# Kernel optimization log

Measured on AMD Instinct MI355X. Metric: run time of the kernel, lower is better.

Reference implementation:

```python
import jax, jax.numpy as jnp
import numpy as np

# Production-scale detection head dims
B_TOTAL = 16      # num_tbins(4) * batch_size(4)
NUM_ANCHORS = 100000
NUM_CLASSES = 8


def setup_inputs() -> dict:
    key = jax.random.key(0)
    k1, k2, k3, k4 = jax.random.split(key, 4)
    # anchors [A,4] = (cx, cy, w, h); widths/heights strictly positive
    ctr = jax.random.uniform(k1, (NUM_ANCHORS, 2), jnp.float32) * 512.0
    wh = jax.random.uniform(k2, (NUM_ANCHORS, 2), jnp.float32) * 64.0 + 8.0
    anchors = jnp.concatenate([ctr, wh], axis=-1)
    loc_preds = jax.random.normal(k3, (B_TOTAL, NUM_ANCHORS, 4), jnp.float32)
    # class scores in [0,1] (post-sigmoid semantics)
    cls_preds = jax.nn.sigmoid(jax.random.normal(k4, (B_TOTAL, NUM_ANCHORS, NUM_CLASSES), jnp.float32))
    return {
        "anchors": anchors,
        "loc_preds": loc_preds,
        "cls_preds": cls_preds,
        "varx": 0.1,
        "vary": 0.2,
        "score_thresh": 0.7,
        "batch_size": 4,
    }


def reference(anchors, loc_preds, cls_preds, varx, vary, score_thresh, batch_size):
    """Anchor decode + score-threshold filtering.

    Faithful to BoxDecoder.forward, but jit-compatible: instead of
    boolean-mask compaction into ragged per-(t,i) lists (data-dependent
    shapes), we return the dense [B*A*C, 6] box tensor plus the keep mask
    and batch_index; (mask, batch_index) fully determine the ragged
    targets[t][i] = box_tensor[mask & (batch_index == t*batch_size+i)].
    """
    B, A, C = cls_preds.shape
    # decode: xy = loc[:2]*varx*anchor_wh + anchor_xy ; wh = exp(loc[2:]*vary)*anchor_wh
    xy = loc_preds[..., :2] * varx * anchors[..., 2:] + anchors[..., :2]
    wh = jnp.exp(loc_preds[..., 2:] * vary) * anchors[..., 2:]
    box_preds = jnp.concatenate([xy - wh * 0.5, xy + wh * 0.5], axis=-1)  # [B,A,4]
    # expand boxes over classes, flatten to [B*A*C, ...] (same order as torch view(-1,...))
    boxes = jnp.broadcast_to(box_preds[:, :, None, :], (B, A, C, 4)).reshape(-1, 4)
    scores = cls_preds.reshape(-1)
    # idxs = b*C + c  ->  label = c+1, batch_index = b
    labels = jnp.broadcast_to(jnp.arange(C, dtype=jnp.float32) + 1.0, (B, A, C)).reshape(-1)
    batch_index = jnp.broadcast_to(jnp.arange(B, dtype=jnp.int32)[:, None, None], (B, A, C)).reshape(-1)
    box_tensor = jnp.concatenate([boxes, scores[:, None], labels[:, None]], axis=1)  # [B*A*C, 6]
    mask = scores >= score_thresh  # keep mask (compaction left to consumer / kernel)
    return box_tensor, mask, batch_index
```

## Files before the change

### kernel.cpp

```cpp
#include <hip/hip_runtime.h>
#include <math.h>


#define MAGIC_SHIFT 38

typedef float vfloat4 __attribute__((ext_vector_type(4)));

__global__ __launch_bounds__(256) void box_decode_pers(
    const vfloat4* __restrict__ anchors,
    const vfloat4* __restrict__ loc,
    const vfloat4* __restrict__ cls4,
    const float*   __restrict__ varx_p,
    const float*   __restrict__ vary_p,
    const float*   __restrict__ th_p,
    vfloat4*       __restrict__ out_box4,
    vfloat4*       __restrict__ out_mask4,
    vfloat4*       __restrict__ out_bidx4,
    unsigned nChunks, unsigned nT, unsigned A,
    unsigned long long invA)
{
    __shared__ vfloat4 s_box[4][64];
    __shared__ vfloat4 s_cls[4][128];

    const unsigned wv   = threadIdx.x >> 6;
    const unsigned lane = threadIdx.x & 63u;
    vfloat4* sbox  = s_box[wv];
    vfloat4* scls4 = s_cls[wv];
    const float* scls = (const float*)scls4;

    const float varx = *varx_p;
    const float vary = *vary_p;
    const float th   = *th_p;

    const unsigned gw = blockIdx.x * 4u + wv;
    const unsigned nw = gridDim.x * 4u;

    for (unsigned ch = gw; ch < nChunks; ch += nw) {
        const unsigned t0     = ch * 64u;
        const unsigned nt_blk = (nT - t0 < 64u) ? (nT - t0) : 64u;

        if (lane < nt_blk) {
            unsigned t = t0 + lane;
            unsigned b = (unsigned)(((unsigned long long)t * invA) >> MAGIC_SHIFT);
            unsigned a = t - b * A;
            vfloat4 anc = anchors[a];
            vfloat4 lp  = loc[t];
            float x = fmaf(lp.x * varx, anc.z, anc.x);
            float y = fmaf(lp.y * varx, anc.w, anc.y);
            float w = expf(lp.z * vary) * anc.z;
            float h = expf(lp.w * vary) * anc.w;
            vfloat4 bx;
            bx.x = fmaf(w, -0.5f, x);
            bx.y = fmaf(h, -0.5f, y);
            bx.z = fmaf(w,  0.5f, x);
            bx.w = fmaf(h,  0.5f, y);
            sbox[lane] = bx;
        }

        const unsigned cbase = t0 * 2u;
        const unsigned clim  = nt_blk * 2u;
        if (lane < clim) {
            vfloat4 c = cls4[cbase + lane];
            scls4[lane] = c;
            vfloat4 m;
            m.x = (c.x >= th) ? 1.0f : 0.0f;
            m.y = (c.y >= th) ? 1.0f : 0.0f;
            m.z = (c.z >= th) ? 1.0f : 0.0f;
            m.w = (c.w >= th) ? 1.0f : 0.0f;
            out_mask4[cbase + lane] = m;
            unsigned tm = t0 + (lane >> 1);
            unsigned bm = (unsigned)(((unsigned long long)tm * invA) >> MAGIC_SHIFT);
            float bf = (float)bm;
            vfloat4 bb = {bf, bf, bf, bf};
            out_bidx4[cbase + lane] = bb;
        }
        {
            unsigned l2 = lane + 64u;
            if (l2 < clim) {
                vfloat4 c = cls4[cbase + l2];
                scls4[l2] = c;
                vfloat4 m;
                m.x = (c.x >= th) ? 1.0f : 0.0f;
                m.y = (c.y >= th) ? 1.0f : 0.0f;
                m.z = (c.z >= th) ? 1.0f : 0.0f;
                m.w = (c.w >= th) ? 1.0f : 0.0f;
                out_mask4[cbase + l2] = m;
                unsigned tm = t0 + 32u + (lane >> 1);
                unsigned bm = (unsigned)(((unsigned long long)tm * invA) >> MAGIC_SHIFT);
                float bf = (float)bm;
                vfloat4 bb = {bf, bf, bf, bf};
                out_bidx4[cbase + l2] = bb;
            }
        }

        asm volatile("s_waitcnt lgkmcnt(0)" ::: "memory");

        const unsigned lim  = nt_blk * 12u;
        const unsigned base = t0 * 12u;
#pragma unroll
        for (unsigned k = 0u; k < 12u; ++k) {
            unsigned lg = k * 64u + lane;
            if (lg < lim) {
                unsigned lt = lg / 12u;
                unsigned j  = lg - lt * 12u;
                unsigned s  = j / 3u;
                unsigned jm = j - s * 3u;
                vfloat4 bx  = sbox[lt];
                float sc0 = scls[lt * 8u + 2u * s];
                float sc1 = scls[lt * 8u + 2u * s + 1u];
                float l0  = (float)(2u * s + 1u);
                float l1  = (float)(2u * s + 2u);
                bool j0 = (jm == 0u);
                bool j1 = (jm == 1u);
                vfloat4 r;
                r.x = j0 ? bx.x : (j1 ? sc0  : bx.z);
                r.y = j0 ? bx.y : (j1 ? l0   : bx.w);
                r.z = j0 ? bx.z : (j1 ? bx.x : sc1);
                r.w = j0 ? bx.w : (j1 ? bx.y : l1);
                out_box4[base + lg] = r;
            }
        }
    }
}

__global__ __launch_bounds__(256) void box_decode_kernel(
    const float4* __restrict__ anchors,
    const float4* __restrict__ loc,
    const float*  __restrict__ cls,
    const float*  __restrict__ varx_p,
    const float*  __restrict__ vary_p,
    const float*  __restrict__ th_p,
    vfloat4*      __restrict__ out_box4,
    float*        __restrict__ out_mask,
    float*        __restrict__ out_bidx,
    unsigned n4, unsigned A, unsigned C, unsigned f4_per_t,
    unsigned long long invA, unsigned long long invF)
{
    unsigned g = blockIdx.x * 256u + threadIdx.x;
    if (g >= n4) return;
    unsigned t  = (unsigned)(((unsigned long long)g * invF) >> MAGIC_SHIFT);
    unsigned j  = g - t * f4_per_t;
    unsigned b  = (unsigned)(((unsigned long long)t * invA) >> MAGIC_SHIFT);
    unsigned a  = t - b * A;
    unsigned s  = j / 3u;
    unsigned jm = j - s * 3u;
    float varx = *varx_p, vary = *vary_p, th = *th_p;
    float4 anc = anchors[a];
    float4 lp  = loc[t];
    float x = fmaf(lp.x * varx, anc.z, anc.x);
    float y = fmaf(lp.y * varx, anc.w, anc.y);
    float w = expf(lp.z * vary) * anc.z;
    float h = expf(lp.w * vary) * anc.w;
    float x1 = fmaf(w, -0.5f, x);
    float y1 = fmaf(h, -0.5f, y);
    float x2 = fmaf(w,  0.5f, x);
    float y2 = fmaf(h,  0.5f, y);
    unsigned r0 = t * C + 2u * s;
    float bf = (float)b;
    vfloat4 r;
    if (jm == 0u) {
        r.x = x1; r.y = y1; r.z = x2; r.w = y2;
    } else if (jm == 1u) {
        float sc0 = cls[r0];
        r.x = sc0; r.y = (float)(2u * s + 1u); r.z = x1; r.w = y1;
        out_mask[r0] = (sc0 >= th) ? 1.0f : 0.0f;
        out_bidx[r0] = bf;
    } else {
        float sc1 = cls[r0 + 1u];
        r.x = x2; r.y = y2; r.z = sc1; r.w = (float)(2u * s + 2u);
        out_mask[r0 + 1u] = (sc1 >= th) ? 1.0f : 0.0f;
        out_bidx[r0 + 1u] = bf;
    }
    out_box4[g] = r;
}

extern "C" void kernel_launch(void* const* d_in, const int* in_sizes, int n_in,
                              void* d_out, int out_size, void* d_ws, size_t ws_size,
                              hipStream_t stream) {
    const float* anchors = (const float*)d_in[0];
    const float* loc     = (const float*)d_in[1];
    const float* cls     = (const float*)d_in[2];
    const float* varx_p  = (const float*)d_in[3];
    const float* vary_p  = (const float*)d_in[4];
    const float* th_p    = (const float*)d_in[5];

    unsigned A = (unsigned)(in_sizes[0] / 4);
    unsigned B = (unsigned)((unsigned)in_sizes[1] / (4u * A));
    unsigned C = (unsigned)((unsigned)in_sizes[2] / (A * B));
    unsigned nT = B * A;
    unsigned rows = nT * C;

    float* out_box  = (float*)d_out;
    float* out_mask = out_box + (size_t)rows * 6;
    float* out_bidx = out_mask + rows;

    unsigned long long invA = ((1ULL << MAGIC_SHIFT) / A) + 1ULL;

    if (C == 8u) {
        unsigned nChunks = (nT + 63u) / 64u;
        unsigned nb = (nChunks + 3u) / 4u;
        if (nb > 2048u) nb = 2048u;
        box_decode_pers<<<dim3(nb), dim3(256), 0, stream>>>(
            (const vfloat4*)anchors, (const vfloat4*)loc, (const vfloat4*)cls,
            varx_p, vary_p, th_p,
            (vfloat4*)out_box, (vfloat4*)out_mask, (vfloat4*)out_bidx,
            nChunks, nT, A, invA);
    } else {
        unsigned f4_per_t = (6u * C) / 4u;
        unsigned n4 = rows * 6u / 4u;
        unsigned long long invF = ((1ULL << MAGIC_SHIFT) / f4_per_t) + 1ULL;
        unsigned nb = (n4 + 255u) / 256u;
        box_decode_kernel<<<dim3(nb), dim3(256), 0, stream>>>(
            (const float4*)anchors, (const float4*)loc, cls,
            varx_p, vary_p, th_p,
            (vfloat4*)out_box, out_mask, out_bidx,
            n4, A, C, f4_per_t, invA, invF);
    }
}
```

Before: 473.0 us.

## Split fused decode kernel into separate box, mask and batch-index kernels

Replaces the single persistent grid-stride kernel, which wrote boxes, mask and batch index together, with three launches: a non-persistent box kernel with one chunk per wave, a mask kernel that rereads the class scores, and a batch-index fill kernel. The intent is simpler per-kernel access patterns and a full-size grid instead of a 2048-block cap. In exchange the class scores are read twice from memory and there are two extra launch overheads on a bandwidth-bound workload.

```diff
diff --git a/kernel.cpp b/kernel.cpp
--- a/kernel.cpp
+++ b/kernel.cpp
@@ -6,16 +6,45 @@
 
 typedef float vfloat4 __attribute__((ext_vector_type(4)));
 
-__global__ __launch_bounds__(256) void box_decode_pers(
+__global__ __launch_bounds__(256) void bidx_kernel(
+    vfloat4* __restrict__ out_bidx4,
+    unsigned nf4, unsigned A,
+    unsigned long long invA)
+{
+    unsigned g = blockIdx.x * 256u + threadIdx.x;
+    if (g >= nf4) return;
+    unsigned t = g >> 1;
+    unsigned b = (unsigned)(((unsigned long long)t * invA) >> MAGIC_SHIFT);
+    float bf = (float)b;
+    vfloat4 v = {bf, bf, bf, bf};
+    out_bidx4[g] = v;
+}
+
+__global__ __launch_bounds__(256) void mask_kernel(
+    const vfloat4* __restrict__ cls4,
+    const float*   __restrict__ th_p,
+    vfloat4*       __restrict__ out_mask4,
+    unsigned nf4)
+{
+    unsigned g = blockIdx.x * 256u + threadIdx.x;
+    if (g >= nf4) return;
+    float th = *th_p;
+    vfloat4 c = cls4[g];
+    vfloat4 m;
+    m.x = (c.x >= th) ? 1.0f : 0.0f;
+    m.y = (c.y >= th) ? 1.0f : 0.0f;
+    m.z = (c.z >= th) ? 1.0f : 0.0f;
+    m.w = (c.w >= th) ? 1.0f : 0.0f;
+    out_mask4[g] = m;
+}
+
+__global__ __launch_bounds__(256) void box_kernel(
     const vfloat4* __restrict__ anchors,
     const vfloat4* __restrict__ loc,
     const vfloat4* __restrict__ cls4,
     const float*   __restrict__ varx_p,
     const float*   __restrict__ vary_p,
-    const float*   __restrict__ th_p,
     vfloat4*       __restrict__ out_box4,
-    vfloat4*       __restrict__ out_mask4,
-    vfloat4*       __restrict__ out_bidx4,
     unsigned nChunks, unsigned nT, unsigned A,
     unsigned long long invA)
 {
@@ -28,97 +57,62 @@
     vfloat4* scls4 = s_cls[wv];
     const float* scls = (const float*)scls4;
 
+    const unsigned ch = blockIdx.x * 4u + wv;
+    if (ch >= nChunks) return;
+    const unsigned t0     = ch * 64u;
+    const unsigned nt_blk = (nT - t0 < 64u) ? (nT - t0) : 64u;
+
     const float varx = *varx_p;
     const float vary = *vary_p;
-    const float th   = *th_p;
-
-    const unsigned gw = blockIdx.x * 4u + wv;
-    const unsigned nw = gridDim.x * 4u;
-
-    for (unsigned ch = gw; ch < nChunks; ch += nw) {
-        const unsigned t0     = ch * 64u;
-        const unsigned nt_blk = (nT - t0 < 64u) ? (nT - t0) : 64u;
-
-        if (lane < nt_blk) {
-            unsigned t = t0 + lane;
-            unsigned b = (unsigned)(((unsigned long long)t * invA) >> MAGIC_SHIFT);
-            unsigned a = t - b * A;
-            vfloat4 anc = anchors[a];
-            vfloat4 lp  = loc[t];
-            float x = fmaf(lp.x * varx, anc.z, anc.x);
-            float y = fmaf(lp.y * varx, anc.w, anc.y);
-            float w = expf(lp.z * vary) * anc.z;
-            float h = expf(lp.w * vary) * anc.w;
-            vfloat4 bx;
-            bx.x = fmaf(w, -0.5f, x);
-            bx.y = fmaf(h, -0.5f, y);
-            bx.z = fmaf(w,  0.5f, x);
-            bx.w = fmaf(h,  0.5f, y);
-            sbox[lane] = bx;
-        }
-
+
+    if (lane < nt_blk) {
+        unsigned t = t0 + lane;
+        unsigned b = (unsigned)(((unsigned long long)t * invA) >> MAGIC_SHIFT);
+        unsigned a = t - b * A;
+        vfloat4 anc = anchors[a];
+        vfloat4 lp  = loc[t];
+        float x = fmaf(lp.x * varx, anc.z, anc.x);
+        float y = fmaf(lp.y * varx, anc.w, anc.y);
+        float w = expf(lp.z * vary) * anc.z;
+        float h = expf(lp.w * vary) * anc.w;
+        vfloat4 bx;
+        bx.x = fmaf(w, -0.5f, x);
+        bx.y = fmaf(h, -0.5f, y);
+        bx.z = fmaf(w,  0.5f, x);
+        bx.w = fmaf(h,  0.5f, y);
+        sbox[lane] = bx;
+    }
+    {
         const unsigned cbase = t0 * 2u;
         const unsigned clim  = nt_blk * 2u;
-        if (lane < clim) {
-            vfloat4 c = cls4[cbase + lane];
-            scls4[lane] = c;
-            vfloat4 m;
-            m.x = (c.x >= th) ? 1.0f : 0.0f;
-            m.y = (c.y >= th) ? 1.0f : 0.0f;
-            m.z = (c.z >= th) ? 1.0f : 0.0f;
-            m.w = (c.w >= th) ? 1.0f : 0.0f;
-            out_mask4[cbase + lane] = m;
-            unsigned tm = t0 + (lane >> 1);
-            unsigned bm = (unsigned)(((unsigned long long)tm * invA) >> MAGIC_SHIFT);
-            float bf = (float)bm;
-            vfloat4 bb = {bf, bf, bf, bf};
-            out_bidx4[cbase + lane] = bb;
-        }
-        {
-            unsigned l2 = lane + 64u;
-            if (l2 < clim) {
-                vfloat4 c = cls4[cbase + l2];
-                scls4[l2] = c;
-                vfloat4 m;
-                m.x = (c.x >= th) ? 1.0f : 0.0f;
-                m.y = (c.y >= th) ? 1.0f : 0.0f;
-                m.z = (c.z >= th) ? 1.0f : 0.0f;
-                m.w = (c.w >= th) ? 1.0f : 0.0f;
-                out_mask4[cbase + l2] = m;
-                unsigned tm = t0 + 32u + (lane >> 1);
-                unsigned bm = (unsigned)(((unsigned long long)tm * invA) >> MAGIC_SHIFT);
-                float bf = (float)bm;
-                vfloat4 bb = {bf, bf, bf, bf};
-                out_bidx4[cbase + l2] = bb;
-            }
-        }
-
-        asm volatile("s_waitcnt lgkmcnt(0)" ::: "memory");
-
-        const unsigned lim  = nt_blk * 12u;
-        const unsigned base = t0 * 12u;
+        if (lane < clim)        scls4[lane]       = cls4[cbase + lane];
+        if (lane + 64u < clim)  scls4[lane + 64u] = cls4[cbase + lane + 64u];
+    }
+    asm volatile("s_waitcnt lgkmcnt(0)" ::: "memory");
+
+    const unsigned lim  = nt_blk * 12u;
+    const unsigned base = t0 * 12u;
 #pragma unroll
-        for (unsigned k = 0u; k < 12u; ++k) {
-            unsigned lg = k * 64u + lane;
-            if (lg < lim) {
-                unsigned lt = lg / 12u;
-                unsigned j  = lg - lt * 12u;
-                unsigned s  = j / 3u;
-                unsigned jm = j - s * 3u;
-                vfloat4 bx  = sbox[lt];
-                float sc0 = scls[lt * 8u + 2u * s];
-                float sc1 = scls[lt * 8u + 2u * s + 1u];
-                float l0  = (float)(2u * s + 1u);
-                float l1  = (float)(2u * s + 2u);
-                bool j0 = (jm == 0u);
-                bool j1 = (jm == 1u);
-                vfloat4 r;
-                r.x = j0 ? bx.x : (j1 ? sc0  : bx.z);
-                r.y = j0 ? bx.y : (j1 ? l0   : bx.w);
-                r.z = j0 ? bx.z : (j1 ? bx.x : sc1);
-                r.w = j0 ? bx.w : (j1 ? bx.y : l1);
-                out_box4[base + lg] = r;
-            }
+    for (unsigned k = 0u; k < 12u; ++k) {
+        unsigned lg = k * 64u + lane;
+        if (lg < lim) {
+            unsigned lt = lg / 12u;
+            unsigned j  = lg - lt * 12u;
+            unsigned s  = j / 3u;
+            unsigned jm = j - s * 3u;
+            vfloat4 bx  = sbox[lt];
+            float sc0 = scls[lt * 8u + 2u * s];
+            float sc1 = scls[lt * 8u + 2u * s + 1u];
+            float l0  = (float)(2u * s + 1u);
+            float l1  = (float)(2u * s + 2u);
+            bool j0 = (jm == 0u);
+            bool j1 = (jm == 1u);
+            vfloat4 r;
+            r.x = j0 ? bx.x : (j1 ? sc0  : bx.z);
+            r.y = j0 ? bx.y : (j1 ? l0   : bx.w);
+            r.z = j0 ? bx.z : (j1 ? bx.x : sc1);
+            r.w = j0 ? bx.w : (j1 ? bx.y : l1);
+            out_box4[base + lg] = r;
         }
     }
 }
@@ -198,13 +192,19 @@
 
     if (C == 8u) {
         unsigned nChunks = (nT + 63u) / 64u;
-        unsigned nb = (nChunks + 3u) / 4u;
-        if (nb > 2048u) nb = 2048u;
-        box_decode_pers<<<dim3(nb), dim3(256), 0, stream>>>(
+        unsigned nbBox   = (nChunks + 3u) / 4u;
+        box_kernel<<<dim3(nbBox), dim3(256), 0, stream>>>(
             (const vfloat4*)anchors, (const vfloat4*)loc, (const vfloat4*)cls,
-            varx_p, vary_p, th_p,
-            (vfloat4*)out_box, (vfloat4*)out_mask, (vfloat4*)out_bidx,
-            nChunks, nT, A, invA);
+            varx_p, vary_p,
+            (vfloat4*)out_box, nChunks, nT, A, invA);
+
+        unsigned nf4 = nT * 2u;
+        unsigned nbM = (nf4 + 255u) / 256u;
+        mask_kernel<<<dim3(nbM), dim3(256), 0, stream>>>(
+            (const vfloat4*)cls, th_p, (vfloat4*)out_mask, nf4);
+
+        bidx_kernel<<<dim3(nbM), dim3(256), 0, stream>>>(
+            (vfloat4*)out_bidx, nf4, A, invA);
     } else {
         unsigned f4_per_t = (6u * C) / 4u;
         unsigned n4 = rows * 6u / 4u;
```

Measured after the change: 477.9 us. No clear change (+1.0%).

## Software-pipeline chunk loads in persistent box decode kernel

Applied to the files above, without the earlier changes.

Restructures the per-wave chunk loop so the next chunk's anchor, loc and class loads are issued into registers before processing the current chunk. This hides global-load latency behind compute and stores. Out-of-range indices are clamped so loads stay unconditional. The grid is resized so each wave handles about four chunks, which raises register use and cuts the number of resident waves.

```diff
diff --git a/kernel.cpp b/kernel.cpp
--- a/kernel.cpp
+++ b/kernel.cpp
@@ -6,7 +6,30 @@
 
 typedef float vfloat4 __attribute__((ext_vector_type(4)));
 
-__global__ __launch_bounds__(256) void box_decode_pers(
+__device__ __forceinline__ unsigned bdiv(unsigned t, unsigned long long invA) {
+    return (unsigned)(((unsigned long long)t * invA) >> MAGIC_SHIFT);
+}
+
+__device__ __forceinline__ void ld_chunk(
+    unsigned ch, unsigned lane, unsigned nT, unsigned A, unsigned long long invA,
+    const vfloat4* __restrict__ anchors, const vfloat4* __restrict__ loc,
+    const vfloat4* __restrict__ cls4,
+    vfloat4& lp, vfloat4& anc, vfloat4& c0, vfloat4& c1)
+{
+    unsigned t0 = ch * 64u;
+    unsigned t  = t0 + lane;  if (t >= nT) t = nT - 1u;
+    unsigned b  = bdiv(t, invA);
+    unsigned a  = t - b * A;
+    anc = anchors[a];
+    lp  = loc[t];
+    unsigned nf4 = nT * 2u;
+    unsigned i0 = t0 * 2u + lane;        if (i0 >= nf4) i0 = nf4 - 1u;
+    unsigned i1 = t0 * 2u + 64u + lane;  if (i1 >= nf4) i1 = nf4 - 1u;
+    c0 = cls4[i0];
+    c1 = cls4[i1];
+}
+
+__global__ __launch_bounds__(256) void box_decode_pipe(
     const vfloat4* __restrict__ anchors,
     const vfloat4* __restrict__ loc,
     const vfloat4* __restrict__ cls4,
@@ -32,19 +55,50 @@
     const float vary = *vary_p;
     const float th   = *th_p;
 
-    const unsigned gw = blockIdx.x * 4u + wv;
     const unsigned nw = gridDim.x * 4u;
-
-    for (unsigned ch = gw; ch < nChunks; ch += nw) {
+    unsigned ch = blockIdx.x * 4u + wv;
+    if (ch >= nChunks) return;
+
+    vfloat4 lp, anc, c0, c1;
+    ld_chunk(ch, lane, nT, A, invA, anchors, loc, cls4, lp, anc, c0, c1);
+
+    for (;;) {
+        const unsigned ch2 = ch + nw;
+        const bool have2 = (ch2 < nChunks);
+        vfloat4 lp2, anc2, c02, c12;
+        if (have2)
+            ld_chunk(ch2, lane, nT, A, invA, anchors, loc, cls4,
+                     lp2, anc2, c02, c12);
+
         const unsigned t0     = ch * 64u;
         const unsigned nt_blk = (nT - t0 < 64u) ? (nT - t0) : 64u;
+        const unsigned cbase  = t0 * 2u;
+        const unsigned clim   = nt_blk * 2u;
+
+        if (lane < clim) {
+            vfloat4 m;
+            m.x = (c0.x >= th) ? 1.0f : 0.0f;
+            m.y = (c0.y >= th) ? 1.0f : 0.0f;
+            m.z = (c0.z >= th) ? 1.0f : 0.0f;
+            m.w = (c0.w >= th) ? 1.0f : 0.0f;
+            out_mask4[cbase + lane] = m;
+            float bf = (float)bdiv(t0 + (lane >> 1), invA);
+            vfloat4 bb = {bf, bf, bf, bf};
+            out_bidx4[cbase + lane] = bb;
+        }
+        if (lane + 64u < clim) {
+            vfloat4 m;
+            m.x = (c1.x >= th) ? 1.0f : 0.0f;
+            m.y = (c1.y >= th) ? 1.0f : 0.0f;
+            m.z = (c1.z >= th) ? 1.0f : 0.0f;
+            m.w = (c1.w >= th) ? 1.0f : 0.0f;
+            out_mask4[cbase + 64u + lane] = m;
+            float bf = (float)bdiv(t0 + 32u + (lane >> 1), invA);
+            vfloat4 bb = {bf, bf, bf, bf};
+            out_bidx4[cbase + 64u + lane] = bb;
+        }
 
         if (lane < nt_blk) {
-            unsigned t = t0 + lane;
-            unsigned b = (unsigned)(((unsigned long long)t * invA) >> MAGIC_SHIFT);
-            unsigned a = t - b * A;
-            vfloat4 anc = anchors[a];
-            vfloat4 lp  = loc[t];
             float x = fmaf(lp.x * varx, anc.z, anc.x);
             float y = fmaf(lp.y * varx, anc.w, anc.y);
             float w = expf(lp.z * vary) * anc.z;
@@ -56,42 +110,8 @@
             bx.w = fmaf(h,  0.5f, y);
             sbox[lane] = bx;
         }
-
-        const unsigned cbase = t0 * 2u;
-        const unsigned clim  = nt_blk * 2u;
-        if (lane < clim) {
-            vfloat4 c = cls4[cbase + lane];
-            scls4[lane] = c;
-            vfloat4 m;
-            m.x = (c.x >= th) ? 1.0f : 0.0f;
-            m.y = (c.y >= th) ? 1.0f : 0.0f;
-            m.z = (c.z >= th) ? 1.0f : 0.0f;
-            m.w = (c.w >= th) ? 1.0f : 0.0f;
-            out_mask4[cbase + lane] = m;
-            unsigned tm = t0 + (lane >> 1);
-            unsigned bm = (unsigned)(((unsigned long long)tm * invA) >> MAGIC_SHIFT);
-            float bf = (float)bm;
-            vfloat4 bb = {bf, bf, bf, bf};
-            out_bidx4[cbase + lane] = bb;
-        }
-        {
-            unsigned l2 = lane + 64u;
-            if (l2 < clim) {
-                vfloat4 c = cls4[cbase + l2];
-                scls4[l2] = c;
-                vfloat4 m;
-                m.x = (c.x >= th) ? 1.0f : 0.0f;
-                m.y = (c.y >= th) ? 1.0f : 0.0f;
-                m.z = (c.z >= th) ? 1.0f : 0.0f;
-                m.w = (c.w >= th) ? 1.0f : 0.0f;
-                out_mask4[cbase + l2] = m;
-                unsigned tm = t0 + 32u + (lane >> 1);
-                unsigned bm = (unsigned)(((unsigned long long)tm * invA) >> MAGIC_SHIFT);
-                float bf = (float)bm;
-                vfloat4 bb = {bf, bf, bf, bf};
-                out_bidx4[cbase + l2] = bb;
-            }
-        }
+        scls4[lane]       = c0;
+        scls4[lane + 64u] = c1;
 
         asm volatile("s_waitcnt lgkmcnt(0)" ::: "memory");
 
@@ -120,6 +140,10 @@
                 out_box4[base + lg] = r;
             }
         }
+
+        if (!have2) break;
+        ch = ch2;
+        lp = lp2; anc = anc2; c0 = c02; c1 = c12;
     }
 }
 
@@ -198,9 +222,8 @@
 
     if (C == 8u) {
         unsigned nChunks = (nT + 63u) / 64u;
-        unsigned nb = (nChunks + 3u) / 4u;
-        if (nb > 2048u) nb = 2048u;
-        box_decode_pers<<<dim3(nb), dim3(256), 0, stream>>>(
+        unsigned nb = (nChunks + 15u) / 16u;
+        box_decode_pipe<<<dim3(nb), dim3(256), 0, stream>>>(
             (const vfloat4*)anchors, (const vfloat4*)loc, (const vfloat4*)cls,
             varx_p, vary_p, th_p,
             (vfloat4*)out_box, (vfloat4*)out_mask, (vfloat4*)out_bidx,
```

Result: no change. 476.1 us (+0.7%).
